# Kernel tuning notes

Hardware: AMD Instinct MI355X
Metric: run time of the kernel (lower is better)

The kernel has to match this reference:

```python
import jax, jax.numpy as jnp
import numpy as np

D = 1024
NS = 12
B = 32
S = 128
K = 512


def setup_inputs() -> dict:
    key = jax.random.key(0)
    ks = jax.random.split(key, 20)
    w = 0.02  # weight scale (xavier-ish)
    return {
        "context": jax.random.normal(ks[0], (B, S, D), jnp.float32),
        "question": jax.random.normal(ks[1], (B, 2 * D), jnp.float32),
        "knowledge": jax.random.normal(ks[2], (B, D, K), jnp.float32),
        "control_init": jax.random.normal(ks[3], (1, 1), jnp.float32),
        # position-aware linears, one per step: Linear(2d, d)
        "pa_w": jax.random.normal(ks[4], (NS, D, 2 * D), jnp.float32) * w,
        "pa_b": jnp.zeros((NS, D), jnp.float32),
        # control unit
        "cq_w": jax.random.normal(ks[5], (D, 2 * D), jnp.float32) * w,
        "cq_b": jnp.zeros((D,), jnp.float32),
        "ca_w": jax.random.normal(ks[6], (1, D), jnp.float32) * w,
        "ca_b": jnp.zeros((1,), jnp.float32),
        # read unit
        "rm_w": jax.random.normal(ks[7], (D, D), jnp.float32) * w,
        "rm_b": jnp.zeros((D,), jnp.float32),
        "ri_w": jax.random.normal(ks[8], (D, 2 * D), jnp.float32) * w,
        "ri_b": jnp.zeros((D,), jnp.float32),
        "ra_w": jax.random.normal(ks[9], (1, D), jnp.float32) * w,
        "ra_b": jnp.zeros((1,), jnp.float32),
        # write unit
        "wm_w": jax.random.normal(ks[10], (D, 2 * D), jnp.float32) * w,
        "wm_b": jnp.zeros((D,), jnp.float32),
    }


def _mac_forward(context, question, knowledge, control_init,
                 pa_w, pa_b, cq_w, cq_b, ca_w, ca_b,
                 rm_w, rm_b, ri_w, ri_b, ra_w, ra_b, wm_w, wm_b):
    b = question.shape[0]
    d = pa_w.shape[1]
    know = jnp.swapaxes(knowledge, 1, 2)  # [B, K, d]
    # all position-aware projections of the question: [n_steps, B, d]
    q_pa_all = jnp.einsum('bq,sdq->sbd', question, pa_w) + pa_b[:, None, :]
    control0 = jnp.broadcast_to(control_init, (b, d))  # randn(1,1).expand(b,d)
    memory0 = q_pa_all[0]

    def step(carry, q_pa):
        control, memory = carry
        # --- control unit ---
        cq = jnp.concatenate([control, q_pa], axis=1) @ cq_w.T + cq_b  # [B, d]
        c_att = jnp.einsum('bsd,d->bs', cq[:, None, :] * context, ca_w[0]) + ca_b[0]
        c_att = jax.nn.softmax(c_att, axis=1)
        new_control = jnp.einsum('bs,bsd->bd', c_att, context)
        # --- read unit ---
        mem_p = memory @ rm_w.T + rm_b  # [B, d]
        inter = mem_p[:, None, :] * know  # [B, K, d]
        inter = jnp.concatenate([inter, know], axis=2) @ ri_w.T + ri_b  # [B, K, d]
        r_att = jnp.einsum('bkd,d->bk', new_control[:, None, :] * inter, ra_w[0]) + ra_b[0]
        r_att = jax.nn.softmax(r_att, axis=1)
        read = jnp.einsum('bk,bkd->bd', r_att, know)
        # --- write unit ---
        new_memory = jnp.concatenate([read, memory], axis=1) @ wm_w.T + wm_b
        return (new_control, new_memory), None

    (control, memory), _ = jax.lax.scan(step, (control0, memory0), q_pa_all)
    return memory


def reference(context, question, knowledge, control_init,
              pa_w, pa_b, cq_w, cq_b, ca_w, ca_b,
              rm_w, rm_b, ri_w, ri_b, ra_w, ra_b, wm_w, wm_b):
    return _mac_forward(context, question, knowledge, control_init,
                        pa_w, pa_b, cq_w, cq_b, ca_w, ca_b,
                        rm_w, rm_b, ri_w, ri_b, ra_w, ra_b, wm_w, wm_b)
```

## Files before the change

### kernel.cpp

```cpp
#include <hip/hip_runtime.h>


#define NSTEP 12

struct GemmArgs {
  const float* X1; long x1g;
  const float* X2; long x2g;
  int c1, c2;
  const float* W; int ldw; long wg;
  const float* bias; long biasg;
  const float* addend; long addg;
  const float* xscale;
  float* out; long outg;
  int N;
};

__global__ __launch_bounds__(256) void gemm32_kernel(GemmArgs a) {
  __shared__ float xs[32 * 512];
  const int g = blockIdx.y;
  const int C = a.c1 + a.c2;
  const float* X1 = a.X1 + (long)g * a.x1g;
  const float* X2 = a.X2 ? a.X2 + (long)g * a.x2g : nullptr;
  const float* W = a.W + (long)g * a.wg;
  const int wave = threadIdx.x >> 6;
  const int lane = threadIdx.x & 63;
  const int n = blockIdx.x * 4 + wave;
  const float* wrow = W + (long)n * a.ldw;
  float acc[32];
#pragma unroll
  for (int b = 0; b < 32; b++) acc[b] = 0.f;

  for (int c0 = 0; c0 < C; c0 += 512) {
    __syncthreads();
#pragma unroll
    for (int i = 0; i < 16; i++) {
      int idx = threadIdx.x + 256 * i;
      int b = idx >> 7;
      int c4 = idx & 127;
      int c = c0 + c4 * 4;
      float4 v;
      if (c < a.c1) v = *(const float4*)(X1 + (long)b * a.c1 + c);
      else          v = *(const float4*)(X2 + (long)b * a.c2 + (c - a.c1));
      if (a.xscale) {
        float4 s = *(const float4*)(a.xscale + c);
        v.x *= s.x; v.y *= s.y; v.z *= s.z; v.w *= s.w;
      }
      *(float4*)(xs + b * 512 + c4 * 4) = v;
    }
    __syncthreads();
#pragma unroll
    for (int i = 0; i < 2; i++) {
      int c = i * 256 + lane * 4;
      float4 wv = *(const float4*)(wrow + c0 + c);
#pragma unroll
      for (int b = 0; b < 32; b++) {
        float4 xv = *(const float4*)(xs + b * 512 + c);
        acc[b] += wv.x * xv.x + wv.y * xv.y + wv.z * xv.z + wv.w * xv.w;
      }
    }
  }
  float res = 0.f;
#pragma unroll
  for (int b = 0; b < 32; b++) {
    float v = acc[b];
#pragma unroll
    for (int off = 32; off; off >>= 1) v += __shfl_xor(v, off, 64);
    if (lane == b) res = v;
  }
  if (lane < 32) {
    float o = res;
    if (a.bias) o += a.bias[(long)g * a.biasg + n];
    if (a.addend) o += a.addend[(long)g * a.addg + (long)lane * a.N + n];
    a.out[(long)g * a.outg + (long)lane * a.N + n] = o;
  }
}

__device__ __forceinline__ void gload_lds16(const float* g, float* l) {
  __builtin_amdgcn_global_load_lds(
      (const __attribute__((address_space(1))) void*)g,
      (__attribute__((address_space(3))) void*)l, 16, 0, 0);
}

__global__ __launch_bounds__(256, 2) void gemm_wide_kernel(GemmArgs a) {
  __shared__ float xs[2][32 * 256];
  const int g = blockIdx.y;
  const int C = a.c1;
  const int nc = C >> 8;
  const float* X1 = a.X1 + (long)g * a.x1g;
  const float* W = a.W + (long)g * a.wg;
  const int wave = threadIdx.x >> 6;
  const int lane = threadIdx.x & 63;
  const int n0 = blockIdx.x * 8 + (wave >> 1) * 4;
  const int bh = (wave & 1) * 16;
  const float* wrow = W + (long)n0 * a.ldw;
  const int cl = lane * 4;

  float acc[64];
#pragma unroll
  for (int v = 0; v < 64; v++) acc[v] = 0.f;

  auto stage = [&](int buf, int c0) {
#pragma unroll
    for (int r = 0; r < 8; r++) {
      int idx = threadIdx.x + 256 * r;
      int b = idx >> 6;
      gload_lds16(X1 + (long)b * C + c0 + (idx & 63) * 4, &xs[buf][idx * 4]);
    }
  };

  stage(0, 0);
  const float* wp0 = wrow + cl;
  float4 wc0 = *(const float4*)(wp0);
  float4 wc1 = *(const float4*)(wp0 + (long)a.ldw);
  float4 wc2 = *(const float4*)(wp0 + 2 * (long)a.ldw);
  float4 wc3 = *(const float4*)(wp0 + 3 * (long)a.ldw);
  __syncthreads();

  for (int i = 0; i < nc; i++) {
    const bool hn = (i + 1) < nc;
    float4 wn0, wn1, wn2, wn3;
    if (hn) {
      const int c0n = (i + 1) << 8;
      stage((i + 1) & 1, c0n);
      const float* wp = wrow + c0n + cl;
      wn0 = *(const float4*)(wp);
      wn1 = *(const float4*)(wp + (long)a.ldw);
      wn2 = *(const float4*)(wp + 2 * (long)a.ldw);
      wn3 = *(const float4*)(wp + 3 * (long)a.ldw);
    }
    const float* xb = &xs[i & 1][0];
#pragma unroll
    for (int b = 0; b < 16; b++) {
      float4 xv = *(const float4*)(xb + (bh + b) * 256 + cl);
      acc[b * 4 + 0] += wc0.x * xv.x + wc0.y * xv.y + wc0.z * xv.z + wc0.w * xv.w;
      acc[b * 4 + 1] += wc1.x * xv.x + wc1.y * xv.y + wc1.z * xv.z + wc1.w * xv.w;
      acc[b * 4 + 2] += wc2.x * xv.x + wc2.y * xv.y + wc2.z * xv.z + wc2.w * xv.w;
      acc[b * 4 + 3] += wc3.x * xv.x + wc3.y * xv.y + wc3.z * xv.z + wc3.w * xv.w;
    }
    if (hn) { wc0 = wn0; wc1 = wn1; wc2 = wn2; wc3 = wn3; }
    __syncthreads();
  }

#pragma unroll
  for (int o = 32; o; o >>= 1) {
    bool up = (lane & o) != 0;
#pragma unroll
    for (int i = 0; i < o; i++) {
      float keep = up ? acc[i + o] : acc[i];
      float send = up ? acc[i] : acc[i + o];
      acc[i] = keep + __shfl_xor(send, o, 64);
    }
  }
  const int bo = bh + (lane >> 2);
  const int nn = n0 + (lane & 3);
  float res = acc[0];
  if (a.bias) res += a.bias[(long)g * a.biasg + nn];
  if (a.addend) res += a.addend[(long)g * a.addg + (long)bo * a.N + nn];
  a.out[(long)g * a.outg + (long)bo * a.N + nn] = res;
}

__global__ __launch_bounds__(1024) void init_control_kernel(const float* ci, float* control) {
  control[blockIdx.x * 1024 + threadIdx.x] = ci[0];
}

__global__ __launch_bounds__(1024) void transpose_kernel(const float* in, float* out) {
  __shared__ float t[32][33];
  int j0 = blockIdx.x * 32;
  int d0 = blockIdx.y * 32;
  int tx = threadIdx.x, ty = threadIdx.y;
  t[ty][tx] = in[(long)(d0 + ty) * 2048 + j0 + tx];
  __syncthreads();
  out[(long)(j0 + ty) * 1024 + d0 + tx] = t[tx][ty];
}

__global__ __launch_bounds__(1024) void ctrl_att_kernel(const float* cq, const float* context,
                                                        const float* ca_w, float* control) {
  int b = blockIdx.x;
  __shared__ float u[1024];
  __shared__ float sc[128];
  int tid = threadIdx.x;
  int wave = tid >> 6, lane = tid & 63;
  u[tid] = cq[b * 1024 + tid] * ca_w[tid];
  __syncthreads();
  const float* ctx = context + (long)b * 128 * 1024;
#pragma unroll
  for (int i = 0; i < 8; i++) {
    int s = wave * 8 + i;
    float v = 0.f;
#pragma unroll
    for (int c = 0; c < 16; c++) v += u[c * 64 + lane] * ctx[(long)s * 1024 + c * 64 + lane];
#pragma unroll
    for (int off = 32; off; off >>= 1) v += __shfl_xor(v, off, 64);
    if (lane == 0) sc[s] = v;
  }
  __syncthreads();
  if (wave == 0) {
    float a0 = sc[lane], a1 = sc[lane + 64];
    float m = fmaxf(a0, a1);
#pragma unroll
    for (int off = 32; off; off >>= 1) m = fmaxf(m, __shfl_xor(m, off, 64));
    float e0 = expf(a0 - m), e1 = expf(a1 - m);
    float s2 = e0 + e1;
#pragma unroll
    for (int off = 32; off; off >>= 1) s2 += __shfl_xor(s2, off, 64);
    float inv = 1.f / s2;
    sc[lane] = e0 * inv;
    sc[lane + 64] = e1 * inv;
  }
  __syncthreads();
  float acc = 0.f;
  for (int s = 0; s < 128; s++) acc += sc[s] * ctx[(long)s * 1024 + tid];
  control[b * 1024 + tid] = acc;
}

__global__ __launch_bounds__(512) void ratt_kernel(const float* knowledge, const float* mem_p,
                                                   const float* h, float* partial) {
  int b = blockIdx.x, jc = blockIdx.y;
  int j0 = jc * 64;
  __shared__ float gl[64];
  if (threadIdx.x < 64) {
    int j = j0 + threadIdx.x;
    gl[threadIdx.x] = mem_p[b * 1024 + j] * h[b * 2048 + j] + h[b * 2048 + 1024 + j];
  }
  __syncthreads();
  int k = threadIdx.x;
  const float* kb = knowledge + ((long)b * 1024 + j0) * 512 + k;
  float acc = 0.f;
#pragma unroll 8
  for (int jj = 0; jj < 64; jj++) acc += gl[jj] * kb[(long)jj * 512];
  partial[((long)jc * 32 + b) * 512 + k] = acc;
}

__global__ __launch_bounds__(256) void read_kernel(const float* partial, const float* knowledge,
                                                   float* readv) {
  int b = blockIdx.x, dg = blockIdx.y;
  __shared__ float aw[512];
  __shared__ float red[4];
  int tid = threadIdx.x;
  int wave = tid >> 6, lane = tid & 63;
  int k0 = tid * 2;
  float r0 = 0.f, r1 = 0.f;
#pragma unroll
  for (int p = 0; p < 16; p++) {
    const float* pp = partial + ((long)p * 32 + b) * 512;
    r0 += pp[k0];
    r1 += pp[k0 + 1];
  }
  float m = fmaxf(r0, r1);
#pragma unroll
  for (int off = 32; off; off >>= 1) m = fmaxf(m, __shfl_xor(m, off, 64));
  if (lane == 0) red[wave] = m;
  __syncthreads();
  m = fmaxf(fmaxf(red[0], red[1]), fmaxf(red[2], red[3]));
  __syncthreads();
  float e0 = expf(r0 - m), e1 = expf(r1 - m);
  float s2 = e0 + e1;
#pragma unroll
  for (int off = 32; off; off >>= 1) s2 += __shfl_xor(s2, off, 64);
  if (lane == 0) red[wave] = s2;
  __syncthreads();
  s2 = red[0] + red[1] + red[2] + red[3];
  float inv = 1.f / s2;
  aw[k0] = e0 * inv;
  aw[k0 + 1] = e1 * inv;
  __syncthreads();
  int d0 = dg * 32 + wave * 8;
  float acc[8];
#pragma unroll
  for (int i = 0; i < 8; i++) acc[i] = 0.f;
  const float* kb = knowledge + ((long)b * 1024 + d0) * 512;
  for (int kc = 0; kc < 8; kc++) {
    int kk = kc * 64 + lane;
    float av = aw[kk];
#pragma unroll
    for (int dd = 0; dd < 8; dd++) acc[dd] += av * kb[(long)dd * 512 + kk];
  }
#pragma unroll
  for (int dd = 0; dd < 8; dd++) {
    float v = acc[dd];
#pragma unroll
    for (int off = 32; off; off >>= 1) v += __shfl_xor(v, off, 64);
    if (lane == dd) readv[b * 1024 + d0 + dd] = v;
  }
}

static inline void launch_gemm(const float* X1, long x1g, const float* X2, long x2g,
                               int c1, int c2, const float* W, int ldw, long wg,
                               const float* bias, long biasg,
                               const float* addend, long addg,
                               const float* xscale, float* out, long outg, int N, int G,
                               hipStream_t stream) {
  GemmArgs a{X1, x1g, X2, x2g, c1, c2, W, ldw, wg, bias, biasg, addend, addg, xscale, out, outg, N};
  gemm32_kernel<<<dim3(N / 4, G), 256, 0, stream>>>(a);
}

static inline void launch_gemm_wide(const float* X1, long x1g, int c1,
                                    const float* W, int ldw, long wg,
                                    const float* bias, long biasg,
                                    float* out, long outg, int N, int G,
                                    hipStream_t stream) {
  GemmArgs a{X1, x1g, nullptr, 0, c1, 0, W, ldw, wg, bias, biasg,
             nullptr, 0, nullptr, out, outg, N};
  gemm_wide_kernel<<<dim3(N / 8, G), 256, 0, stream>>>(a);
}

extern "C" void kernel_launch(void* const* d_in, const int* in_sizes, int n_in,
                              void* d_out, int out_size, void* d_ws, size_t ws_size,
                              hipStream_t stream) {
  const float* context      = (const float*)d_in[0];
  const float* question     = (const float*)d_in[1];
  const float* knowledge    = (const float*)d_in[2];
  const float* control_init = (const float*)d_in[3];
  const float* pa_w = (const float*)d_in[4];
  const float* pa_b = (const float*)d_in[5];
  const float* cq_w = (const float*)d_in[6];
  const float* cq_b = (const float*)d_in[7];
  const float* ca_w = (const float*)d_in[8];
  const float* rm_w = (const float*)d_in[10];
  const float* rm_b = (const float*)d_in[11];
  const float* ri_w = (const float*)d_in[12];
  const float* ra_w = (const float*)d_in[14];
  const float* wm_w = (const float*)d_in[16];
  const float* wm_b = (const float*)d_in[17];
  float* out = (float*)d_out;

  float* p = (float*)d_ws;
  float* q_pa_all = p; p += NSTEP * 32 * 1024;
  float* qc_all   = p; p += NSTEP * 32 * 1024;
  float* ri_wT    = p; p += 2048 * 1024;
  float* control  = p; p += 32 * 1024;
  float* mem0     = p; p += 32 * 1024;
  float* mem1     = p; p += 32 * 1024;
  float* cq       = p; p += 32 * 1024;
  float* mem_p    = p; p += 32 * 1024;
  float* h        = p; p += 32 * 2048;
  float* partial  = p; p += 16 * 32 * 512;
  float* readv    = p; p += 32 * 1024;

  init_control_kernel<<<32, 1024, 0, stream>>>(control_init, control);
  transpose_kernel<<<dim3(64, 32), dim3(32, 32), 0, stream>>>(ri_w, ri_wT);
  launch_gemm_wide(question, 0, 2048, pa_w, 2048, 1024L * 2048,
                   pa_b, 1024, q_pa_all, 32 * 1024, 1024, NSTEP, stream);
  hipMemcpyAsync(mem0, q_pa_all, 32 * 1024 * sizeof(float), hipMemcpyDeviceToDevice, stream);
  launch_gemm_wide(q_pa_all, 32 * 1024, 1024, cq_w + 1024, 2048, 0,
                   nullptr, 0, qc_all, 32 * 1024, 1024, NSTEP, stream);

  float* mems[2] = {mem0, mem1};
  for (int s = 0; s < NSTEP; s++) {
    float* mo = mems[s & 1];
    float* mn = (s == NSTEP - 1) ? out : mems[(s + 1) & 1];
    launch_gemm(control, 0, nullptr, 0, 1024, 0, cq_w, 2048, 0,
                cq_b, 0, qc_all + (long)s * 32 * 1024, 0, nullptr, cq, 0, 1024, 1, stream);
    launch_gemm(mo, 0, nullptr, 0, 1024, 0, rm_w, 1024, 0,
                rm_b, 0, nullptr, 0, nullptr, mem_p, 0, 1024, 1, stream);
    ctrl_att_kernel<<<32, 1024, 0, stream>>>(cq, context, ca_w, control);
    launch_gemm(control, 0, nullptr, 0, 1024, 0, ri_wT, 1024, 0,
                nullptr, 0, nullptr, 0, ra_w, h, 0, 2048, 1, stream);
    ratt_kernel<<<dim3(32, 16), 512, 0, stream>>>(knowledge, mem_p, h, partial);
    read_kernel<<<dim3(32, 32), 256, 0, stream>>>(partial, knowledge, readv);
    launch_gemm(readv, 0, mo, 0, 1024, 1024, wm_w, 2048, 0,
                wm_b, 0, nullptr, 0, nullptr, mn, 0, 1024, 1, stream);
  }
}
```

Measured before the change: 1.560 ms.

## Fuse per-step MAC kernels into one persistent cooperative kernel with grid syncs

Replaces the seven kernel launches per recurrence step with a single cooperative persistent kernel of 256 blocks, each phase separated by grid.sync(). The cq and rm_w GEMMs run concurrently on disjoint block halves, and control attention is split into a score phase and a weighted-sum phase so more blocks take part. This targets launch overhead and inter-kernel gaps across 84 small launches, at the cost of grid-wide barriers and a fixed block count per phase.

```diff
diff --git a/kernel.cpp b/kernel.cpp
--- a/kernel.cpp
+++ b/kernel.cpp
@@ -1,7 +1,10 @@
 #include <hip/hip_runtime.h>
+#include <hip/hip_cooperative_groups.h>
 
 
 #define NSTEP 12
+
+namespace cg = cooperative_groups;
 
 struct GemmArgs {
   const float* X1; long x1g;
@@ -14,66 +17,6 @@
   float* out; long outg;
   int N;
 };
-
-__global__ __launch_bounds__(256) void gemm32_kernel(GemmArgs a) {
-  __shared__ float xs[32 * 512];
-  const int g = blockIdx.y;
-  const int C = a.c1 + a.c2;
-  const float* X1 = a.X1 + (long)g * a.x1g;
-  const float* X2 = a.X2 ? a.X2 + (long)g * a.x2g : nullptr;
-  const float* W = a.W + (long)g * a.wg;
-  const int wave = threadIdx.x >> 6;
-  const int lane = threadIdx.x & 63;
-  const int n = blockIdx.x * 4 + wave;
-  const float* wrow = W + (long)n * a.ldw;
-  float acc[32];
-#pragma unroll
-  for (int b = 0; b < 32; b++) acc[b] = 0.f;
-
-  for (int c0 = 0; c0 < C; c0 += 512) {
-    __syncthreads();
-#pragma unroll
-    for (int i = 0; i < 16; i++) {
-      int idx = threadIdx.x + 256 * i;
-      int b = idx >> 7;
-      int c4 = idx & 127;
-      int c = c0 + c4 * 4;
-      float4 v;
-      if (c < a.c1) v = *(const float4*)(X1 + (long)b * a.c1 + c);
-      else          v = *(const float4*)(X2 + (long)b * a.c2 + (c - a.c1));
-      if (a.xscale) {
-        float4 s = *(const float4*)(a.xscale + c);
-        v.x *= s.x; v.y *= s.y; v.z *= s.z; v.w *= s.w;
-      }
-      *(float4*)(xs + b * 512 + c4 * 4) = v;
-    }
-    __syncthreads();
-#pragma unroll
-    for (int i = 0; i < 2; i++) {
-      int c = i * 256 + lane * 4;
-      float4 wv = *(const float4*)(wrow + c0 + c);
-#pragma unroll
-      for (int b = 0; b < 32; b++) {
-        float4 xv = *(const float4*)(xs + b * 512 + c);
-        acc[b] += wv.x * xv.x + wv.y * xv.y + wv.z * xv.z + wv.w * xv.w;
-      }
-    }
-  }
-  float res = 0.f;
-#pragma unroll
-  for (int b = 0; b < 32; b++) {
-    float v = acc[b];
-#pragma unroll
-    for (int off = 32; off; off >>= 1) v += __shfl_xor(v, off, 64);
-    if (lane == b) res = v;
-  }
-  if (lane < 32) {
-    float o = res;
-    if (a.bias) o += a.bias[(long)g * a.biasg + n];
-    if (a.addend) o += a.addend[(long)g * a.addg + (long)lane * a.N + n];
-    a.out[(long)g * a.outg + (long)lane * a.N + n] = o;
-  }
-}
 
 __device__ __forceinline__ void gload_lds16(const float* g, float* l) {
   __builtin_amdgcn_global_load_lds(
@@ -155,7 +98,6 @@
   const int nn = n0 + (lane & 3);
   float res = acc[0];
   if (a.bias) res += a.bias[(long)g * a.biasg + nn];
-  if (a.addend) res += a.addend[(long)g * a.addg + (long)bo * a.N + nn];
   a.out[(long)g * a.outg + (long)bo * a.N + nn] = res;
 }
 
@@ -173,125 +115,231 @@
   out[(long)(j0 + ty) * 1024 + d0 + tx] = t[tx][ty];
 }
 
-__global__ __launch_bounds__(1024) void ctrl_att_kernel(const float* cq, const float* context,
-                                                        const float* ca_w, float* control) {
-  int b = blockIdx.x;
-  __shared__ float u[1024];
-  __shared__ float sc[128];
-  int tid = threadIdx.x;
-  int wave = tid >> 6, lane = tid & 63;
-  u[tid] = cq[b * 1024 + tid] * ca_w[tid];
-  __syncthreads();
-  const float* ctx = context + (long)b * 128 * 1024;
-#pragma unroll
-  for (int i = 0; i < 8; i++) {
-    int s = wave * 8 + i;
-    float v = 0.f;
-#pragma unroll
-    for (int c = 0; c < 16; c++) v += u[c * 64 + lane] * ctx[(long)s * 1024 + c * 64 + lane];
+
+struct MacArgs {
+  const float* context;
+  const float* knowledge;
+  const float* cq_w; const float* cq_b;
+  const float* ca_w;
+  const float* rm_w; const float* rm_b;
+  const float* ri_wT; const float* ra_w;
+  const float* wm_w; const float* wm_b;
+  const float* qc_all;
+  float* control; float* mem0; float* mem1;
+  float* cq; float* mem_p; float* h;
+  float* partial; float* readv; float* scg;
+  float* outp;
+};
+
+__device__ __forceinline__ void gemm_phase(
+    float* xs, const float* X1, const float* X2, int c1, int c2,
+    const float* W, int ldw, const float* bias, const float* addend,
+    const float* xscale, float* out, int N, int nblk,
+    int wave, int lane, int t) {
+  const int C = c1 + c2;
+  const int n = nblk * 8 + wave;
+  const float* wrow = W + (long)n * ldw;
+  float acc[32];
+#pragma unroll
+  for (int b = 0; b < 32; b++) acc[b] = 0.f;
+  for (int c0 = 0; c0 < C; c0 += 512) {
+    __syncthreads();
+#pragma unroll
+    for (int i = 0; i < 8; i++) {
+      int idx = t + 512 * i;
+      int b = idx >> 7;
+      int c4 = idx & 127;
+      int c = c0 + c4 * 4;
+      float4 v;
+      if (c < c1) v = *(const float4*)(X1 + (long)b * c1 + c);
+      else        v = *(const float4*)(X2 + (long)b * c2 + (c - c1));
+      if (xscale) {
+        float4 s4 = *(const float4*)(xscale + c);
+        v.x *= s4.x; v.y *= s4.y; v.z *= s4.z; v.w *= s4.w;
+      }
+      *(float4*)(xs + b * 512 + c4 * 4) = v;
+    }
+    __syncthreads();
+#pragma unroll
+    for (int i = 0; i < 2; i++) {
+      int c = i * 256 + lane * 4;
+      float4 wv = *(const float4*)(wrow + c0 + c);
+#pragma unroll
+      for (int b = 0; b < 32; b++) {
+        float4 xv = *(const float4*)(xs + b * 512 + c);
+        acc[b] += wv.x * xv.x + wv.y * xv.y + wv.z * xv.z + wv.w * xv.w;
+      }
+    }
+  }
+  float res = 0.f;
+#pragma unroll
+  for (int b = 0; b < 32; b++) {
+    float v = acc[b];
 #pragma unroll
     for (int off = 32; off; off >>= 1) v += __shfl_xor(v, off, 64);
-    if (lane == 0) sc[s] = v;
-  }
-  __syncthreads();
-  if (wave == 0) {
-    float a0 = sc[lane], a1 = sc[lane + 64];
-    float m = fmaxf(a0, a1);
-#pragma unroll
-    for (int off = 32; off; off >>= 1) m = fmaxf(m, __shfl_xor(m, off, 64));
-    float e0 = expf(a0 - m), e1 = expf(a1 - m);
-    float s2 = e0 + e1;
-#pragma unroll
-    for (int off = 32; off; off >>= 1) s2 += __shfl_xor(s2, off, 64);
-    float inv = 1.f / s2;
-    sc[lane] = e0 * inv;
-    sc[lane + 64] = e1 * inv;
-  }
-  __syncthreads();
-  float acc = 0.f;
-  for (int s = 0; s < 128; s++) acc += sc[s] * ctx[(long)s * 1024 + tid];
-  control[b * 1024 + tid] = acc;
-}
-
-__global__ __launch_bounds__(512) void ratt_kernel(const float* knowledge, const float* mem_p,
-                                                   const float* h, float* partial) {
-  int b = blockIdx.x, jc = blockIdx.y;
-  int j0 = jc * 64;
-  __shared__ float gl[64];
-  if (threadIdx.x < 64) {
-    int j = j0 + threadIdx.x;
-    gl[threadIdx.x] = mem_p[b * 1024 + j] * h[b * 2048 + j] + h[b * 2048 + 1024 + j];
-  }
-  __syncthreads();
-  int k = threadIdx.x;
-  const float* kb = knowledge + ((long)b * 1024 + j0) * 512 + k;
-  float acc = 0.f;
+    if (lane == b) res = v;
+  }
+  if (lane < 32) {
+    float o = res;
+    if (bias) o += bias[n];
+    if (addend) o += addend[(long)lane * N + n];
+    out[(long)lane * N + n] = o;
+  }
+}
+
+__global__ __launch_bounds__(512, 2) void mac_loop_kernel(MacArgs A) {
+  cg::grid_group grid = cg::this_grid();
+  __shared__ float smem[16384];
+  const int p = blockIdx.x;
+  const int t = threadIdx.x;
+  const int wave = t >> 6, lane = t & 63;
+
+  const float* mo = A.mem0;
+  float* mnbuf = A.mem1;
+
+  for (int s = 0; s < NSTEP; s++) {
+    float* mn = (s == NSTEP - 1) ? A.outp : mnbuf;
+
+    if (p < 128)
+      gemm_phase(smem, A.control, nullptr, 1024, 0, A.cq_w, 2048, A.cq_b,
+                 A.qc_all + (long)s * 32 * 1024, nullptr, A.cq, 1024, p,
+                 wave, lane, t);
+    else
+      gemm_phase(smem, mo, nullptr, 1024, 0, A.rm_w, 1024, A.rm_b,
+                 nullptr, nullptr, A.mem_p, 1024, p - 128, wave, lane, t);
+    grid.sync();
+
+    {
+      int b = p >> 3, sg = p & 7;
+      float* u = smem;
+      u[t] = A.cq[b * 1024 + t] * A.ca_w[t];
+      u[t + 512] = A.cq[b * 1024 + t + 512] * A.ca_w[t + 512];
+      __syncthreads();
+#pragma unroll
+      for (int i = 0; i < 2; i++) {
+        int s2 = sg * 16 + wave * 2 + i;
+        const float* cr = A.context + (long)b * 128 * 1024 + (long)s2 * 1024;
+        float v = 0.f;
+#pragma unroll
+        for (int c = 0; c < 16; c++) v += u[c * 64 + lane] * cr[c * 64 + lane];
+#pragma unroll
+        for (int off = 32; off; off >>= 1) v += __shfl_xor(v, off, 64);
+        if (lane == 0) A.scg[b * 128 + s2] = v;
+      }
+    }
+    grid.sync();
+
+    {
+      int b = p >> 3, dq = p & 7;
+      float* sw = smem;
+      float* ew = smem + 128;
+      float* red = smem + 256;
+      if (t < 128) sw[t] = A.scg[b * 128 + t];
+      __syncthreads();
+      float m = sw[0];
+      for (int s2 = 1; s2 < 128; s2++) m = fmaxf(m, sw[s2]);
+      if (t < 128) ew[t] = expf(sw[t] - m);
+      __syncthreads();
+      float Z = 0.f;
+      for (int s2 = 0; s2 < 128; s2++) Z += ew[s2];
+      float invZ = 1.f / Z;
+      int d = dq * 128 + (t & 127);
+      int q = t >> 7;
+      const float* ctx = A.context + (long)b * 128 * 1024;
+      float acc = 0.f;
+      for (int s2 = q * 32; s2 < q * 32 + 32; s2++)
+        acc += ew[s2] * ctx[(long)s2 * 1024 + d];
+      red[q * 128 + (t & 127)] = acc;
+      __syncthreads();
+      if (t < 128) {
+        float v = red[t] + red[128 + t] + red[256 + t] + red[384 + t];
+        A.control[b * 1024 + dq * 128 + t] = v * invZ;
+      }
+    }
+    grid.sync();
+
+    gemm_phase(smem, A.control, nullptr, 1024, 0, A.ri_wT, 1024, nullptr,
+               nullptr, A.ra_w, A.h, 2048, p, wave, lane, t);
+    grid.sync();
+
+    {
+      float* gl = smem;
+      for (int r = 0; r < 2; r++) {
+        int T = p * 2 + r, b = T >> 4, jc = T & 15, j0 = jc * 64;
+        if (r) __syncthreads();
+        if (t < 64)
+          gl[t] = A.mem_p[b * 1024 + j0 + t] * A.h[b * 2048 + j0 + t] +
+                  A.h[b * 2048 + 1024 + j0 + t];
+        __syncthreads();
+        const float* kb = A.knowledge + ((long)b * 1024 + j0) * 512 + t;
+        float acc = 0.f;
 #pragma unroll 8
-  for (int jj = 0; jj < 64; jj++) acc += gl[jj] * kb[(long)jj * 512];
-  partial[((long)jc * 32 + b) * 512 + k] = acc;
-}
-
-__global__ __launch_bounds__(256) void read_kernel(const float* partial, const float* knowledge,
-                                                   float* readv) {
-  int b = blockIdx.x, dg = blockIdx.y;
-  __shared__ float aw[512];
-  __shared__ float red[4];
-  int tid = threadIdx.x;
-  int wave = tid >> 6, lane = tid & 63;
-  int k0 = tid * 2;
-  float r0 = 0.f, r1 = 0.f;
-#pragma unroll
-  for (int p = 0; p < 16; p++) {
-    const float* pp = partial + ((long)p * 32 + b) * 512;
-    r0 += pp[k0];
-    r1 += pp[k0 + 1];
-  }
-  float m = fmaxf(r0, r1);
-#pragma unroll
-  for (int off = 32; off; off >>= 1) m = fmaxf(m, __shfl_xor(m, off, 64));
-  if (lane == 0) red[wave] = m;
-  __syncthreads();
-  m = fmaxf(fmaxf(red[0], red[1]), fmaxf(red[2], red[3]));
-  __syncthreads();
-  float e0 = expf(r0 - m), e1 = expf(r1 - m);
-  float s2 = e0 + e1;
-#pragma unroll
-  for (int off = 32; off; off >>= 1) s2 += __shfl_xor(s2, off, 64);
-  if (lane == 0) red[wave] = s2;
-  __syncthreads();
-  s2 = red[0] + red[1] + red[2] + red[3];
-  float inv = 1.f / s2;
-  aw[k0] = e0 * inv;
-  aw[k0 + 1] = e1 * inv;
-  __syncthreads();
-  int d0 = dg * 32 + wave * 8;
-  float acc[8];
-#pragma unroll
-  for (int i = 0; i < 8; i++) acc[i] = 0.f;
-  const float* kb = knowledge + ((long)b * 1024 + d0) * 512;
-  for (int kc = 0; kc < 8; kc++) {
-    int kk = kc * 64 + lane;
-    float av = aw[kk];
-#pragma unroll
-    for (int dd = 0; dd < 8; dd++) acc[dd] += av * kb[(long)dd * 512 + kk];
-  }
-#pragma unroll
-  for (int dd = 0; dd < 8; dd++) {
-    float v = acc[dd];
-#pragma unroll
-    for (int off = 32; off; off >>= 1) v += __shfl_xor(v, off, 64);
-    if (lane == dd) readv[b * 1024 + d0 + dd] = v;
-  }
-}
-
-static inline void launch_gemm(const float* X1, long x1g, const float* X2, long x2g,
-                               int c1, int c2, const float* W, int ldw, long wg,
-                               const float* bias, long biasg,
-                               const float* addend, long addg,
-                               const float* xscale, float* out, long outg, int N, int G,
-                               hipStream_t stream) {
-  GemmArgs a{X1, x1g, X2, x2g, c1, c2, W, ldw, wg, bias, biasg, addend, addg, xscale, out, outg, N};
-  gemm32_kernel<<<dim3(N / 4, G), 256, 0, stream>>>(a);
+        for (int jj = 0; jj < 64; jj++) acc += gl[jj] * kb[(long)jj * 512];
+        A.partial[((long)jc * 32 + b) * 512 + t] = acc;
+      }
+    }
+    grid.sync();
+
+    {
+      float* aw = smem;
+      float* red8 = smem + 512;
+      for (int r = 0; r < 2; r++) {
+        int T = p * 2 + r, b = T >> 4, dg = T & 15;
+        if (r) __syncthreads();
+        float rk = 0.f;
+#pragma unroll
+        for (int pp = 0; pp < 16; pp++)
+          rk += A.partial[((long)pp * 32 + b) * 512 + t];
+        float m = rk;
+#pragma unroll
+        for (int off = 32; off; off >>= 1) m = fmaxf(m, __shfl_xor(m, off, 64));
+        if (lane == 0) red8[wave] = m;
+        __syncthreads();
+        m = red8[0];
+        for (int q = 1; q < 8; q++) m = fmaxf(m, red8[q]);
+        __syncthreads();
+        float e = expf(rk - m);
+        float zz = e;
+#pragma unroll
+        for (int off = 32; off; off >>= 1) zz += __shfl_xor(zz, off, 64);
+        if (lane == 0) red8[wave] = zz;
+        __syncthreads();
+        float Z = 0.f;
+        for (int q = 0; q < 8; q++) Z += red8[q];
+        aw[t] = e / Z;
+        __syncthreads();
+        int d0 = dg * 64 + wave * 8;
+        float acc8[8];
+#pragma unroll
+        for (int dd = 0; dd < 8; dd++) acc8[dd] = 0.f;
+        const float* kb = A.knowledge + ((long)b * 1024 + d0) * 512;
+#pragma unroll
+        for (int kc = 0; kc < 8; kc++) {
+          int kk = kc * 64 + lane;
+          float av = aw[kk];
+#pragma unroll
+          for (int dd = 0; dd < 8; dd++) acc8[dd] += av * kb[(long)dd * 512 + kk];
+        }
+#pragma unroll
+        for (int dd = 0; dd < 8; dd++) {
+          float v = acc8[dd];
+#pragma unroll
+          for (int off = 32; off; off >>= 1) v += __shfl_xor(v, off, 64);
+          if (lane == dd) A.readv[b * 1024 + d0 + dd] = v;
+        }
+      }
+    }
+    grid.sync();
+
+    if (p < 128)
+      gemm_phase(smem, A.readv, mo, 1024, 1024, A.wm_w, 2048, A.wm_b,
+                 nullptr, nullptr, mn, 1024, p, wave, lane, t);
+    grid.sync();
+
+    if (s < NSTEP - 1) {
+      const float* tmp = mo; mo = mnbuf; mnbuf = (float*)tmp;
+    }
+  }
 }
 
 static inline void launch_gemm_wide(const float* X1, long x1g, int c1,
@@ -336,6 +384,7 @@
   float* h        = p; p += 32 * 2048;
   float* partial  = p; p += 16 * 32 * 512;
   float* readv    = p; p += 32 * 1024;
+  float* scg      = p; p += 32 * 128;
 
   init_control_kernel<<<32, 1024, 0, stream>>>(control_init, control);
   transpose_kernel<<<dim3(64, 32), dim3(32, 32), 0, stream>>>(ri_w, ri_wT);
@@ -345,20 +394,10 @@
   launch_gemm_wide(q_pa_all, 32 * 1024, 1024, cq_w + 1024, 2048, 0,
                    nullptr, 0, qc_all, 32 * 1024, 1024, NSTEP, stream);
 
-  float* mems[2] = {mem0, mem1};
-  for (int s = 0; s < NSTEP; s++) {
-    float* mo = mems[s & 1];
-    float* mn = (s == NSTEP - 1) ? out : mems[(s + 1) & 1];
-    launch_gemm(control, 0, nullptr, 0, 1024, 0, cq_w, 2048, 0,
-                cq_b, 0, qc_all + (long)s * 32 * 1024, 0, nullptr, cq, 0, 1024, 1, stream);
-    launch_gemm(mo, 0, nullptr, 0, 1024, 0, rm_w, 1024, 0,
-                rm_b, 0, nullptr, 0, nullptr, mem_p, 0, 1024, 1, stream);
-    ctrl_att_kernel<<<32, 1024, 0, stream>>>(cq, context, ca_w, control);
-    launch_gemm(control, 0, nullptr, 0, 1024, 0, ri_wT, 1024, 0,
-                nullptr, 0, nullptr, 0, ra_w, h, 0, 2048, 1, stream);
-    ratt_kernel<<<dim3(32, 16), 512, 0, stream>>>(knowledge, mem_p, h, partial);
-    read_kernel<<<dim3(32, 32), 256, 0, stream>>>(partial, knowledge, readv);
-    launch_gemm(readv, 0, mo, 0, 1024, 1024, wm_w, 2048, 0,
-                wm_b, 0, nullptr, 0, nullptr, mn, 0, 1024, 1, stream);
-  }
-}
+  MacArgs A{context, knowledge, cq_w, cq_b, ca_w, rm_w, rm_b, ri_wT, ra_w,
+            wm_w, wm_b, qc_all, control, mem0, mem1, cq, mem_p, h,
+            partial, readv, scg, out};
+  void* kargs[] = {(void*)&A};
+  hipLaunchCooperativeKernel((const void*)mac_loop_kernel, dim3(256), dim3(512),
+                             kargs, 0, stream);
+}
```

After: 4.924 ms. 3.16x slower.

## Merge independent per-step kernels into combined launches to cut launch count

Applied to the files above, without the earlier changes.

Fuses the memory projection GEMM with the control-attention kernel into one launch that splits work by block index. Computes the next step's control-question GEMM alongside the read-input GEMM in a dual launch, hoisting the first one before the loop. This cuts seven launches per step to five and lets independent work share the GPU. The memory GEMM in the fused kernel now uses 1024-thread blocks with a different tiling, and an unused addend path is removed from the wide GEMM.

```diff
diff --git a/kernel.cpp b/kernel.cpp
--- a/kernel.cpp
+++ b/kernel.cpp
@@ -15,7 +15,7 @@
   int N;
 };
 
-__global__ __launch_bounds__(256) void gemm32_kernel(GemmArgs a) {
+__device__ __forceinline__ void gemm32_body(const GemmArgs& a, int bx) {
   __shared__ float xs[32 * 512];
   const int g = blockIdx.y;
   const int C = a.c1 + a.c2;
@@ -24,7 +24,7 @@
   const float* W = a.W + (long)g * a.wg;
   const int wave = threadIdx.x >> 6;
   const int lane = threadIdx.x & 63;
-  const int n = blockIdx.x * 4 + wave;
+  const int n = bx * 4 + wave;
   const float* wrow = W + (long)n * a.ldw;
   float acc[32];
 #pragma unroll
@@ -75,6 +75,16 @@
   }
 }
 
+__global__ __launch_bounds__(256) void gemm32_kernel(GemmArgs a) {
+  gemm32_body(a, blockIdx.x);
+}
+
+__global__ __launch_bounds__(256) void gemm32_dual_kernel(GemmArgs a0, GemmArgs a1, int split) {
+  int bx = blockIdx.x;
+  if (bx < split) gemm32_body(a0, bx);
+  else            gemm32_body(a1, bx - split);
+}
+
 __device__ __forceinline__ void gload_lds16(const float* g, float* l) {
   __builtin_amdgcn_global_load_lds(
       (const __attribute__((address_space(1))) void*)g,
@@ -155,7 +165,6 @@
   const int nn = n0 + (lane & 3);
   float res = acc[0];
   if (a.bias) res += a.bias[(long)g * a.biasg + nn];
-  if (a.addend) res += a.addend[(long)g * a.addg + (long)bo * a.N + nn];
   a.out[(long)g * a.outg + (long)bo * a.N + nn] = res;
 }
 
@@ -173,44 +182,94 @@
   out[(long)(j0 + ty) * 1024 + d0 + tx] = t[tx][ty];
 }
 
-__global__ __launch_bounds__(1024) void ctrl_att_kernel(const float* cq, const float* context,
-                                                        const float* ca_w, float* control) {
-  int b = blockIdx.x;
-  __shared__ float u[1024];
-  __shared__ float sc[128];
-  int tid = threadIdx.x;
-  int wave = tid >> 6, lane = tid & 63;
-  u[tid] = cq[b * 1024 + tid] * ca_w[tid];
-  __syncthreads();
-  const float* ctx = context + (long)b * 128 * 1024;
-#pragma unroll
-  for (int i = 0; i < 8; i++) {
-    int s = wave * 8 + i;
-    float v = 0.f;
-#pragma unroll
-    for (int c = 0; c < 16; c++) v += u[c * 64 + lane] * ctx[(long)s * 1024 + c * 64 + lane];
-#pragma unroll
-    for (int off = 32; off; off >>= 1) v += __shfl_xor(v, off, 64);
-    if (lane == 0) sc[s] = v;
-  }
-  __syncthreads();
-  if (wave == 0) {
-    float a0 = sc[lane], a1 = sc[lane + 64];
-    float m = fmaxf(a0, a1);
-#pragma unroll
-    for (int off = 32; off; off >>= 1) m = fmaxf(m, __shfl_xor(m, off, 64));
-    float e0 = expf(a0 - m), e1 = expf(a1 - m);
-    float s2 = e0 + e1;
-#pragma unroll
-    for (int off = 32; off; off >>= 1) s2 += __shfl_xor(s2, off, 64);
-    float inv = 1.f / s2;
-    sc[lane] = e0 * inv;
-    sc[lane + 64] = e1 * inv;
-  }
-  __syncthreads();
-  float acc = 0.f;
-  for (int s = 0; s < 128; s++) acc += sc[s] * ctx[(long)s * 1024 + tid];
-  control[b * 1024 + tid] = acc;
+__global__ __launch_bounds__(1024) void ctrl_g2_kernel(GemmArgs g2,
+                                                       const float* cq,
+                                                       const float* context,
+                                                       const float* ca_w,
+                                                       float* control) {
+  __shared__ float smem[32 * 512];
+  const int bx = blockIdx.x;
+  const int t = threadIdx.x;
+  const int wave = t >> 6, lane = t & 63;
+
+  if (bx < 64) {
+    const float* X1 = g2.X1;
+    const int C = g2.c1;
+    const int n = bx * 16 + wave;
+    const float* wrow = g2.W + (long)n * g2.ldw;
+    float acc[32];
+#pragma unroll
+    for (int b = 0; b < 32; b++) acc[b] = 0.f;
+    for (int c0 = 0; c0 < C; c0 += 512) {
+      __syncthreads();
+#pragma unroll
+      for (int i = 0; i < 4; i++) {
+        int idx = t + 1024 * i;
+        int b = idx >> 7, c4 = idx & 127;
+        *(float4*)(smem + b * 512 + c4 * 4) =
+            *(const float4*)(X1 + (long)b * C + c0 + c4 * 4);
+      }
+      __syncthreads();
+#pragma unroll
+      for (int i = 0; i < 2; i++) {
+        int c = i * 256 + lane * 4;
+        float4 wv = *(const float4*)(wrow + c0 + c);
+#pragma unroll
+        for (int b = 0; b < 32; b++) {
+          float4 xv = *(const float4*)(smem + b * 512 + c);
+          acc[b] += wv.x * xv.x + wv.y * xv.y + wv.z * xv.z + wv.w * xv.w;
+        }
+      }
+    }
+    float res = 0.f;
+#pragma unroll
+    for (int b = 0; b < 32; b++) {
+      float v = acc[b];
+#pragma unroll
+      for (int off = 32; off; off >>= 1) v += __shfl_xor(v, off, 64);
+      if (lane == b) res = v;
+    }
+    if (lane < 32) {
+      float o = res;
+      if (g2.bias) o += g2.bias[n];
+      g2.out[(long)lane * g2.N + n] = o;
+    }
+  } else {
+    const int b = bx - 64;
+    float* u = smem;
+    float* sc = smem + 1024;
+    u[t] = cq[b * 1024 + t] * ca_w[t];
+    __syncthreads();
+    const float* ctx = context + (long)b * 128 * 1024;
+#pragma unroll
+    for (int i = 0; i < 8; i++) {
+      int s2 = wave * 8 + i;
+      float v = 0.f;
+#pragma unroll
+      for (int c = 0; c < 16; c++) v += u[c * 64 + lane] * ctx[(long)s2 * 1024 + c * 64 + lane];
+#pragma unroll
+      for (int off = 32; off; off >>= 1) v += __shfl_xor(v, off, 64);
+      if (lane == 0) sc[s2] = v;
+    }
+    __syncthreads();
+    if (wave == 0) {
+      float a0 = sc[lane], a1 = sc[lane + 64];
+      float m = fmaxf(a0, a1);
+#pragma unroll
+      for (int off = 32; off; off >>= 1) m = fmaxf(m, __shfl_xor(m, off, 64));
+      float e0 = expf(a0 - m), e1 = expf(a1 - m);
+      float s2 = e0 + e1;
+#pragma unroll
+      for (int off = 32; off; off >>= 1) s2 += __shfl_xor(s2, off, 64);
+      float inv = 1.f / s2;
+      sc[lane] = e0 * inv;
+      sc[lane + 64] = e1 * inv;
+    }
+    __syncthreads();
+    float acc = 0.f;
+    for (int s2 = 0; s2 < 128; s2++) acc += sc[s2] * ctx[(long)s2 * 1024 + t];
+    control[b * 1024 + t] = acc;
+  }
 }
 
 __global__ __launch_bounds__(512) void ratt_kernel(const float* knowledge, const float* mem_p,
@@ -282,16 +341,6 @@
     for (int off = 32; off; off >>= 1) v += __shfl_xor(v, off, 64);
     if (lane == dd) readv[b * 1024 + d0 + dd] = v;
   }
-}
-
-static inline void launch_gemm(const float* X1, long x1g, const float* X2, long x2g,
-                               int c1, int c2, const float* W, int ldw, long wg,
-                               const float* bias, long biasg,
-                               const float* addend, long addg,
-                               const float* xscale, float* out, long outg, int N, int G,
-                               hipStream_t stream) {
-  GemmArgs a{X1, x1g, X2, x2g, c1, c2, W, ldw, wg, bias, biasg, addend, addg, xscale, out, outg, N};
-  gemm32_kernel<<<dim3(N / 4, G), 256, 0, stream>>>(a);
 }
 
 static inline void launch_gemm_wide(const float* X1, long x1g, int c1,
@@ -345,20 +394,42 @@
   launch_gemm_wide(q_pa_all, 32 * 1024, 1024, cq_w + 1024, 2048, 0,
                    nullptr, 0, qc_all, 32 * 1024, 1024, NSTEP, stream);
 
+  {
+    GemmArgs g1{control, 0, nullptr, 0, 1024, 0, cq_w, 2048, 0,
+                cq_b, 0, qc_all, 0, nullptr, cq, 0, 1024};
+    gemm32_kernel<<<256, 256, 0, stream>>>(g1);
+  }
+
   float* mems[2] = {mem0, mem1};
   for (int s = 0; s < NSTEP; s++) {
     float* mo = mems[s & 1];
     float* mn = (s == NSTEP - 1) ? out : mems[(s + 1) & 1];
-    launch_gemm(control, 0, nullptr, 0, 1024, 0, cq_w, 2048, 0,
-                cq_b, 0, qc_all + (long)s * 32 * 1024, 0, nullptr, cq, 0, 1024, 1, stream);
-    launch_gemm(mo, 0, nullptr, 0, 1024, 0, rm_w, 1024, 0,
-                rm_b, 0, nullptr, 0, nullptr, mem_p, 0, 1024, 1, stream);
-    ctrl_att_kernel<<<32, 1024, 0, stream>>>(cq, context, ca_w, control);
-    launch_gemm(control, 0, nullptr, 0, 1024, 0, ri_wT, 1024, 0,
-                nullptr, 0, nullptr, 0, ra_w, h, 0, 2048, 1, stream);
+
+    {
+      GemmArgs g2{mo, 0, nullptr, 0, 1024, 0, rm_w, 1024, 0,
+                  rm_b, 0, nullptr, 0, nullptr, mem_p, 0, 1024};
+      ctrl_g2_kernel<<<96, 1024, 0, stream>>>(g2, cq, context, ca_w, control);
+    }
+
+    {
+      GemmArgs g3{control, 0, nullptr, 0, 1024, 0, ri_wT, 1024, 0,
+                  nullptr, 0, nullptr, 0, ra_w, h, 0, 2048};
+      if (s < NSTEP - 1) {
+        GemmArgs g1{control, 0, nullptr, 0, 1024, 0, cq_w, 2048, 0,
+                    cq_b, 0, qc_all + (long)(s + 1) * 32 * 1024, 0, nullptr,
+                    cq, 0, 1024};
+        gemm32_dual_kernel<<<768, 256, 0, stream>>>(g3, g1, 512);
+      } else {
+        gemm32_kernel<<<512, 256, 0, stream>>>(g3);
+      }
+    }
+
     ratt_kernel<<<dim3(32, 16), 512, 0, stream>>>(knowledge, mem_p, h, partial);
     read_kernel<<<dim3(32, 32), 256, 0, stream>>>(partial, knowledge, readv);
-    launch_gemm(readv, 0, mo, 0, 1024, 1024, wm_w, 2048, 0,
-                wm_b, 0, nullptr, 0, nullptr, mn, 0, 1024, 1, stream);
-  }
-}
+    {
+      GemmArgs g6{readv, 0, mo, 0, 1024, 1024, wm_w, 2048, 0,
+                  wm_b, 0, nullptr, 0, nullptr, mn, 0, 1024};
+      gemm32_kernel<<<256, 256, 0, stream>>>(g6);
+    }
+  }
+}
```

Measured after the change: 1.410 ms. -9.6%, faster.
